# Performance work log

Measured on AMD Instinct MI355X. Metric: run time of the kernel, lower is better.

Reference implementation:

```python
import jax, jax.numpy as jnp
import numpy as np
import math

E = 65536        # neighbor pairs (edges)
NAT = 2048       # atoms
NRAD = 24        # radial basis size
ZETA = [1, 2, 3, 4]
NCOMP = len(ZETA) + 1  # radial components: one 2-body + one per zeta
RCUT = 6.0
NELEM = 94       # one-hot element encoding size
EMB = 16         # species embedding dim


def _tables():
    """Static lxlylz enumeration per zeta: triples with lx+ly+lz = n, n in 0..z,
    multinomial/binomial normalization and (-1)^n lambda sign."""
    f = np.vectorize(math.factorial)
    tabs = []
    for z in ZETA:
        L = []
        for n in range(z + 1):
            for lx in range(n + 1):
                for ly in range(n - lx + 1):
                    L.append((lx, ly, n - lx - ly))
        L = np.array(L, np.int64)              # [K,3]
        nsum = L.sum(1)                        # [K]
        fact_lxlylz = f(L[:, 0]) * f(L[:, 1]) * f(L[:, 2])
        # (nfact/fact_lxlylz) * z!/((z-n)! n!) = z! / ((z-n)! * lx!ly!lz!)
        fact_norm = math.factorial(z) / (f(z - nsum) * fact_lxlylz)
        lam = (-1.0) ** nsum
        tabs.append((jnp.asarray(L, jnp.float32),
                     jnp.asarray(fact_norm, jnp.float32),
                     jnp.asarray(lam, jnp.float32)))
    return tabs

TABS = _tables()


def _forward(rij, Wr1, br1, Wr2, br2, Ws1, bs1, Ws2, bs2,
             Wa1, ba1, Wa2, ba2, Wa3, ba3, first_atom_idx, species_idx):
    nat = species_idx.shape[0]
    r = jnp.linalg.norm(rij, axis=1)                       # [E]
    u = rij / r[:, None]                                   # [E,3] unit vectors
    fc = 0.5 * (jnp.cos(jnp.pi * jnp.minimum(r, RCUT) / RCUT) + 1.0)
    centers = jnp.linspace(0.0, RCUT, NRAD, dtype=jnp.float32)
    width = RCUT / NRAD
    basis = jnp.exp(-((r[:, None] - centers) ** 2) / (2.0 * width * width)) * fc[:, None]  # [E,NRAD]
    # learned radial functions -> [E, NRAD, NCOMP]
    h = jax.nn.silu(basis @ Wr1 + br1)
    radial = jax.nn.silu(h @ Wr2 + br2).reshape(-1, NRAD, NCOMP)
    seg = first_atom_idx
    # two-body descriptor
    feats = [jax.ops.segment_sum(radial[:, :, 0], seg, num_segments=nat)]  # [nat,NRAD]
    for iz, z in enumerate(ZETA):
        L, fnorm, lam = TABS[iz]
        # g_ij over lxlylz combos: prod of powers of unit-vector components
        g_ij = jnp.prod((u[:, None, :] + 1e-12) ** L[None, :, :], axis=-1) * fnorm  # [E,K]
        g = jnp.einsum('er,ek->erk', radial[:, :, iz + 1], g_ij)                    # [E,NRAD,K]
        gi = jax.ops.segment_sum(g, seg, num_segments=nat)                          # [nat,NRAD,K]
        g2 = gi * gi
        norm = 2.0 ** (1.0 - z)
        feats.append(jnp.sum(g2, axis=-1) * norm)          # lambda = +1
        feats.append(jnp.sum(g2 * lam, axis=-1) * norm)    # lambda = -1
    feat = jnp.concatenate(feats, axis=1)                  # [nat, NRAD*(1+2*nzeta)]
    # species embedding and correlation
    onehot = jax.nn.one_hot(species_idx, NELEM, dtype=feat.dtype)
    emb = jax.nn.silu(onehot @ Ws1 + bs1) @ Ws2 + bs2      # [nat,EMB]
    x = (feat[:, :, None] * emb[:, None, :]).reshape(nat, -1)  # [nat, F*EMB]
    h = jax.nn.silu(x @ Wa1 + ba1)
    h = jax.nn.silu(h @ Wa2 + ba2)
    e = h @ Wa3 + ba3                                      # [nat,1] atomic energies
    return jnp.sum(e)                                      # total energy


def setup_inputs() -> dict:
    key = jax.random.key(0)
    ks = jax.random.split(key, 12)
    def w(k, shp):
        return jax.random.normal(k, shp, jnp.float32) / np.float32(np.sqrt(shp[0]))
    F = NRAD * (1 + 2 * len(ZETA)) * EMB  # 3456
    return {
        "rij": jax.random.normal(ks[0], (E, 3), jnp.float32) * 2.0,
        "Wr1": w(ks[1], (NRAD, 64)), "br1": jnp.zeros((64,), jnp.float32),
        "Wr2": w(ks[2], (64, NCOMP * NRAD)), "br2": jnp.zeros((NCOMP * NRAD,), jnp.float32),
        "Ws1": w(ks[3], (NELEM, 32)), "bs1": jnp.zeros((32,), jnp.float32),
        "Ws2": w(ks[4], (32, EMB)), "bs2": jnp.zeros((EMB,), jnp.float32),
        "Wa1": w(ks[5], (F, 256)), "ba1": jnp.zeros((256,), jnp.float32),
        "Wa2": w(ks[6], (256, 128)), "ba2": jnp.zeros((128,), jnp.float32),
        "Wa3": w(ks[7], (128, 1)), "ba3": jnp.zeros((1,), jnp.float32),
        "first_atom_idx": jnp.sort(jax.random.randint(ks[8], (E,), 0, NAT)),
        "species_idx": jax.random.randint(ks[9], (NAT,), 0, NELEM),
    }


def reference(rij, Wr1, br1, Wr2, br2, Ws1, bs1, Ws2, bs2,
              Wa1, ba1, Wa2, ba2, Wa3, ba3, first_atom_idx, species_idx):
    return _forward(rij, Wr1, br1, Wr2, br2, Ws1, bs1, Ws2, bs2,
                    Wa1, ba1, Wa2, ba2, Wa3, ba3, first_atom_idx, species_idx)
```

## Files before the change

### kernel.cpp

```cpp
#include <hip/hip_runtime.h>
#include <math.h>

#define KTOT 69
#define NRADC 24
#define NFEAT 216
#define NELEMC 94
#define EMBC 16
#define H1C 256
#define H2C 128
#define CE 16
#define EPR 20
#define KGN 18
#define GSTR 84
#define GISTR 76

__device__ __constant__ int c_lx[KTOT] = {
  0,0,0,1,
  0,0,0,1,0,0,0,1,1,2,
  0,0,0,1,0,0,0,1,1,2,0,0,0,0,1,1,1,2,2,3,
  0,0,0,1,0,0,0,1,1,2,0,0,0,0,1,1,1,2,2,3,0,0,0,0,0,1,1,1,1,2,2,2,3,3,4};
__device__ __constant__ int c_ly[KTOT] = {
  0,0,1,0,
  0,0,1,0,0,1,2,0,1,0,
  0,0,1,0,0,1,2,0,1,0,0,1,2,3,0,1,2,0,1,0,
  0,0,1,0,0,1,2,0,1,0,0,1,2,3,0,1,2,0,1,0,0,1,2,3,4,0,1,2,3,0,1,2,0,1,0};
__device__ __constant__ int c_lz[KTOT] = {
  0,1,0,0,
  0,1,0,0,2,1,0,1,0,0,
  0,1,0,0,2,1,0,1,0,0,3,2,1,0,2,1,0,1,0,0,
  0,1,0,0,2,1,0,1,0,0,3,2,1,0,2,1,0,1,0,0,4,3,2,1,0,3,2,1,0,2,1,0,1,0,0};
__device__ __constant__ float c_fn[KTOT] = {
  1,1,1,1,
  1,2,2,2,1,2,1,2,2,1,
  1,3,3,3,3,6,3,6,6,3,1,3,3,1,3,6,3,3,3,1,
  1,4,4,4,6,12,6,12,12,6,4,12,12,4,12,24,12,12,12,4,
  1,4,6,4,1,4,12,12,4,6,12,6,4,4,1};
__device__ __constant__ float c_lam[KTOT] = {
  1,-1,-1,-1,
  1,-1,-1,-1,1,1,1,1,1,1,
  1,-1,-1,-1,1,1,1,1,1,1,-1,-1,-1,-1,-1,-1,-1,-1,-1,-1,
  1,-1,-1,-1,1,1,1,1,1,1,-1,-1,-1,-1,-1,-1,-1,-1,-1,-1,
  1,1,1,1,1,1,1,1,1,1,1,1,1,1,1};
__device__ __constant__ int c_k0[4] = {0,4,14,34};
__device__ __constant__ int c_kn[4] = {4,10,20,35};
__device__ __constant__ float c_zn[4] = {1.0f, 0.5f, 0.25f, 0.125f};
__device__ __constant__ int c_zidg[KGN] = {0, 1,1,1, 2,2,2,2,2, 3,3,3,3,3,3,3,3,3};

__device__ __forceinline__ float silu(float x) { return x / (1.0f + expf(-x)); }
__device__ __forceinline__ float4 silu4(float4 v) {
  v.x = silu(v.x); v.y = silu(v.y); v.z = silu(v.z); v.w = silu(v.w); return v;
}
__device__ __forceinline__ void fma4(float4& a, float s, const float4 w) {
  a.x += s * w.x; a.y += s * w.y; a.z += s * w.z; a.w += s * w.w;
}
__device__ __forceinline__ void fma44(float4& a, const float4 x, const float4 y) {
  a.x += x.x * y.x; a.y += x.y * y.y; a.z += x.z * y.z; a.w += x.w * y.w;
}
__device__ __forceinline__ float hsum4(const float4 v) { return (v.x + v.y) + (v.z + v.w); }
__device__ __forceinline__ float powsel(int l, float p, float p2, float p3, float p4) {
  float v = 1.0f;
  v = l >= 1 ? p : v;
  v = l >= 2 ? p2 : v;
  v = l >= 3 ? p3 : v;
  v = l >= 4 ? p4 : v;
  return v;
}

__global__ __launch_bounds__(256) void k_prep(
    const int* __restrict__ fai, const int* __restrict__ spc,
    const float* __restrict__ Ws1, const float* __restrict__ bs1,
    const float* __restrict__ Ws2, const float* __restrict__ bs2,
    const float* __restrict__ Wa1,
    int* __restrict__ bounds, int* __restrict__ order,
    float* __restrict__ B, int E, int nat, int nbB) {
  const int blk = blockIdx.x;
  const int tid = threadIdx.x;
  __shared__ float s_hh[24 * 32];
  __shared__ float s_emb[24 * EMBC];
  __shared__ int s_cnt[NELEMC];
  __shared__ int s_off[NELEMC];

  if (blk < nbB) {
    int e = blk * 256 + tid;
    if (e < E) {
      int f = fai[e];
      int fp = (e == 0) ? -1 : fai[e - 1];
      for (int a = fp + 1; a <= f; ++a) bounds[a] = e;
      if (e == E - 1)
        for (int a = f + 1; a <= nat; ++a) bounds[a] = E;
    }
  } else if (blk == nbB) {
    for (int i = tid; i < NELEMC; i += 256) s_cnt[i] = 0;
    __syncthreads();
    for (int a = tid; a < nat; a += 256) atomicAdd(&s_cnt[spc[a]], 1);
    __syncthreads();
    if (tid == 0) {
      int run = 0;
      for (int s = 0; s < NELEMC; ++s) { s_off[s] = run; run += s_cnt[s]; }
    }
    __syncthreads();
    for (int a = tid; a < nat; a += 256) {
      int pos = atomicAdd(&s_off[spc[a]], 1);
      order[pos] = a;
    }
  } else {
    const int bi = blk - nbB - 1;
    const int i = bi >> 2;
    const int sc0 = (bi & 3) * 24;
    const int scn = min(NELEMC, sc0 + 24) - sc0;
    const int o = tid;
    for (int idx = tid; idx < scn * 32; idx += 256) {
      int s = idx >> 5, c = idx & 31;
      s_hh[idx] = silu(Ws1[(sc0 + s) * 32 + c] + bs1[c]);
    }
    __syncthreads();
    for (int idx = tid; idx < scn * EMBC; idx += 256) {
      int s = idx >> 4, j = idx & 15;
      float acc = bs2[j];
      #pragma unroll
      for (int c = 0; c < 32; ++c) acc += s_hh[s * 32 + c] * Ws2[c * EMBC + j];
      s_emb[idx] = acc;
    }
    __syncthreads();
    float w[EMBC];
    #pragma unroll
    for (int j = 0; j < EMBC; ++j) w[j] = Wa1[(size_t)(i * EMBC + j) * H1C + o];
    for (int s = 0; s < scn; ++s) {
      float acc = 0.0f;
      #pragma unroll
      for (int j = 0; j < EMBC; ++j) acc += s_emb[s * EMBC + j] * w[j];
      B[((size_t)(sc0 + s) * NFEAT + i) * H1C + o] = acc;
    }
  }
}

template <int NQ>
__device__ __forceinline__ void edge_l2(
    const float* __restrict__ s_h, const float* __restrict__ Wr2,
    const float* __restrict__ br2, float4* __restrict__ radial4,
    int lane, int og, int ebase, int E) {
  float4 a0[NQ], a1[NQ];
  const float4* b2 = (const float4*)(br2 + og * 32);
  #pragma unroll
  for (int q = 0; q < NQ; ++q) { a0[q] = b2[q]; a1[q] = b2[q]; }
  #pragma unroll 2
  for (int j = 0; j < 64; ++j) {
    float h0 = s_h[lane * 65 + j];
    float h1 = s_h[(lane + 64) * 65 + j];
    const float4* w = (const float4*)(Wr2 + j * 120 + og * 32);
    #pragma unroll
    for (int q = 0; q < NQ; ++q) {
      float4 wq = w[q];
      fma4(a0[q], h0, wq);
      fma4(a1[q], h1, wq);
    }
  }
  const int e0 = ebase + lane, e1 = e0 + 64;
  if (e0 < E) {
    #pragma unroll
    for (int q = 0; q < NQ; ++q) radial4[e0 * 30 + og * 8 + q] = silu4(a0[q]);
  }
  if (e1 < E) {
    #pragma unroll
    for (int q = 0; q < NQ; ++q) radial4[e1 * 30 + og * 8 + q] = silu4(a1[q]);
  }
}

__global__ __launch_bounds__(256) void k_edge(
    const float* __restrict__ rij,
    const float* __restrict__ Wr1, const float* __restrict__ br1,
    const float* __restrict__ Wr2, const float* __restrict__ br2,
    float4* __restrict__ radial4, int E) {
  __shared__ float s_bas[128 * 25];
  __shared__ float s_h[128 * 65];
  const int tid = threadIdx.x;
  const int lane = tid & 63;
  const int og = __builtin_amdgcn_readfirstlane(tid >> 6);
  const int ebase = blockIdx.x * 128;

  {
    const int ehh = og >> 1;
    const int m0 = (og & 1) * 12;
    const int el = ehh * 64 + lane;
    const int eg = ebase + el;
    float x = 0.0f, y = 0.0f, z = 0.0f;
    const bool ev = eg < E;
    if (ev) { x = rij[3 * eg]; y = rij[3 * eg + 1]; z = rij[3 * eg + 2]; }
    float r = sqrtf(x * x + y * y + z * z);
    float fcv = ev ? 0.5f * (cosf(3.14159265358979323846f * fminf(r, 6.0f) *
                                  (1.0f / 6.0f)) + 1.0f)
                   : 0.0f;
    #pragma unroll
    for (int t = 0; t < 12; ++t) {
      int m = m0 + t;
      float d = r - (6.0f / 23.0f) * (float)m;
      s_bas[el * 25 + m] = expf(-8.0f * d * d) * fcv;
    }
  }
  __syncthreads();

  {
    const float4* b1 = (const float4*)(br1 + og * 16);
    float4 c0[4], c1[4];
    #pragma unroll
    for (int q = 0; q < 4; ++q) { c0[q] = b1[q]; c1[q] = b1[q]; }
    #pragma unroll 4
    for (int m = 0; m < NRADC; ++m) {
      float bA = s_bas[lane * 25 + m];
      float bB = s_bas[(lane + 64) * 25 + m];
      const float4* w = (const float4*)(Wr1 + m * 64 + og * 16);
      #pragma unroll
      for (int q = 0; q < 4; ++q) {
        float4 wq = w[q];
        fma4(c0[q], bA, wq);
        fma4(c1[q], bB, wq);
      }
    }
    #pragma unroll
    for (int q = 0; q < 4; ++q) {
      float4 v0 = silu4(c0[q]), v1 = silu4(c1[q]);
      int b0 = lane * 65 + og * 16 + 4 * q;
      int b1o = (lane + 64) * 65 + og * 16 + 4 * q;
      s_h[b0 + 0] = v0.x; s_h[b0 + 1] = v0.y; s_h[b0 + 2] = v0.z; s_h[b0 + 3] = v0.w;
      s_h[b1o + 0] = v1.x; s_h[b1o + 1] = v1.y; s_h[b1o + 2] = v1.z; s_h[b1o + 3] = v1.w;
    }
  }
  __syncthreads();

  if (og < 3) edge_l2<8>(s_h, Wr2, br2, radial4, lane, og, ebase, E);
  else        edge_l2<6>(s_h, Wr2, br2, radial4, lane, og, ebase, E);
}

__global__ __launch_bounds__(256) void k_atom(
    const float* __restrict__ rij,
    const float4* __restrict__ radial4,
    const int* __restrict__ bounds,
    float* __restrict__ feat, int E) {
  const int a = blockIdx.x;
  const int tid = threadIdx.x;
  __shared__ __align__(16) float s_radT[120 * EPR];
  __shared__ __align__(16) float s_gijT[KGN * GSTR];
  __shared__ __align__(16) float s_gi[NRADC * GISTR];
  __shared__ float s_feat[NFEAT];

  const int start = bounds[a];
  const int end = bounds[a + 1];

  const int e = tid & 15;
  const int sub = tid >> 4;

  const bool is_tile = tid < 216;
  const int eh = (tid < 216) ? (tid / 108) : 0;
  const int tile = (tid < 216) ? (tid % 108) : 0;
  const int rg = tile % 6;
  const int kg = tile / 6;
  const int comp0 = rg * 20 + 1 + c_zidg[kg];
  const bool is_2b = (tid >= 216 && tid < 240);
  const int rad2b = tid - 216;

  const int kstart = sub < 5 ? sub * 5 : 25 + (sub - 5) * 4;
  const int kcnt = sub < 5 ? 5 : 4;
  int t_pk[5], t_addr[5]; float t_fn[5];
  #pragma unroll
  for (int t = 0; t < 5; ++t) {
    int k = (t < kcnt) ? kstart + t : 0;
    t_pk[t] = c_lx[k] | (c_ly[k] << 8) | (c_lz[k] << 16);
    t_fn[t] = c_fn[k];
    int prow = k + (k < 14 ? 0 : 2);
    t_addr[t] = (prow >> 2) * GSTR + (prow & 3) * EPR + e;
  }

  const int pe0 = tid / 30, pc0 = tid - pe0 * 30;
  const int pe1 = (tid + 256) / 30, pc1 = (tid + 256) - pe1 * 30;

  if (tid < 60) {
    int rr = tid / EPR, ec = tid % EPR;
    int fkg = rr < 2 ? 3 : 17;
    int fj = rr < 2 ? 2 + rr : 3;
    s_gijT[fkg * GSTR + fj * EPR + ec] = 0.0f;
  }

  float4 acc[4][4];
  #pragma unroll
  for (int i = 0; i < 4; ++i)
    #pragma unroll
    for (int j = 0; j < 4; ++j) acc[i][j] = make_float4(0, 0, 0, 0);
  float4 acc2b = make_float4(0, 0, 0, 0);

  float4 pfA, pfB;
  float rx, ry, rz;
  auto prefetch = [&](int c0) {
    int lim = (end - c0) * 30;
    pfA = make_float4(0, 0, 0, 0);
    pfB = make_float4(0, 0, 0, 0);
    if (tid < lim) pfA = radial4[(size_t)c0 * 30 + tid];
    if (tid < 224 && tid + 256 < lim) pfB = radial4[(size_t)c0 * 30 + 256 + tid];
    int eg = c0 + e;
    rx = 0.0f; ry = 0.0f; rz = 0.0f;
    if (eg < end) { rx = rij[3 * eg]; ry = rij[3 * eg + 1]; rz = rij[3 * eg + 2]; }
  };
  prefetch(start);

  for (int c0 = start; c0 < end; c0 += CE) {
    __syncthreads();
    {
      int c = pc0 * 4;
      s_radT[(c + 0) * EPR + pe0] = pfA.x;
      s_radT[(c + 1) * EPR + pe0] = pfA.y;
      s_radT[(c + 2) * EPR + pe0] = pfA.z;
      s_radT[(c + 3) * EPR + pe0] = pfA.w;
      if (tid < 224) {
        int c2 = pc1 * 4;
        s_radT[(c2 + 0) * EPR + pe1] = pfB.x;
        s_radT[(c2 + 1) * EPR + pe1] = pfB.y;
        s_radT[(c2 + 2) * EPR + pe1] = pfB.z;
        s_radT[(c2 + 3) * EPR + pe1] = pfB.w;
      }
    }
    {
      const bool ev = (c0 + e) < end;
      float r = sqrtf(rx * rx + ry * ry + rz * rz);
      float inv = 1.0f / r;
      float px = rx * inv + 1e-12f, py = ry * inv + 1e-12f, pz = rz * inv + 1e-12f;
      float p2x = px * px, p3x = p2x * px, p4x = p2x * p2x;
      float p2y = py * py, p3y = p2y * py, p4y = p2y * p2y;
      float p2z = pz * pz, p3z = p2z * pz, p4z = p2z * p2z;
      #pragma unroll
      for (int t = 0; t < 5; ++t) {
        if (t < kcnt) {
          int pk = t_pk[t];
          float g = powsel(pk & 0xff, px, p2x, p3x, p4x) *
                    powsel((pk >> 8) & 0xff, py, p2y, p3y, p4y) *
                    powsel(pk >> 16, pz, p2z, p3z, p4z) * t_fn[t];
          s_gijT[t_addr[t]] = ev ? g : 0.0f;
        }
      }
    }
    __syncthreads();
    prefetch(c0 + CE);
    if (is_tile) {
      #pragma unroll
      for (int s = 0; s < 2; ++s) {
        int e0 = eh * 8 + s * 4;
        float4 gg[4];
        #pragma unroll
        for (int j = 0; j < 4; ++j)
          gg[j] = *(const float4*)&s_gijT[kg * GSTR + j * EPR + e0];
        #pragma unroll
        for (int i = 0; i < 4; ++i) {
          float4 rr = *(const float4*)&s_radT[(comp0 + 5 * i) * EPR + e0];
          #pragma unroll
          for (int j = 0; j < 4; ++j) fma44(acc[i][j], rr, gg[j]);
        }
      }
    }
    if (is_2b) {
      #pragma unroll
      for (int e0 = 0; e0 < 16; e0 += 4) {
        float4 v = *(const float4*)&s_radT[(rad2b * 5) * EPR + e0];
        acc2b.x += v.x; acc2b.y += v.y; acc2b.z += v.z; acc2b.w += v.w;
      }
    }
  }

  float4 hs[4];
  #pragma unroll
  for (int i = 0; i < 4; ++i)
    hs[i] = make_float4(hsum4(acc[i][0]), hsum4(acc[i][1]),
                        hsum4(acc[i][2]), hsum4(acc[i][3]));
  __syncthreads();
  if (is_tile && eh == 0) {
    #pragma unroll
    for (int i = 0; i < 4; ++i)
      *(float4*)&s_gi[(rg * 4 + i) * GISTR + kg * 4] = hs[i];
  }
  if (is_2b) s_feat[rad2b] = hsum4(acc2b);
  __syncthreads();
  if (is_tile && eh == 1) {
    #pragma unroll
    for (int i = 0; i < 4; ++i) {
      float4 v = *(const float4*)&s_gi[(rg * 4 + i) * GISTR + kg * 4];
      v.x += hs[i].x; v.y += hs[i].y; v.z += hs[i].z; v.w += hs[i].w;
      *(float4*)&s_gi[(rg * 4 + i) * GISTR + kg * 4] = v;
    }
  }
  __syncthreads();

  if (tid < 192) {
    int zb = tid / NRADC;
    int rad = tid - zb * NRADC;
    int z = zb >> 1;
    bool neg = zb & 1;
    int k0 = c_k0[z], kn = c_kn[z];
    float s = 0.0f;
    for (int k = k0; k < k0 + kn; ++k) {
      int prow = k + (k < 14 ? 0 : 2);
      float g = s_gi[rad * GISTR + prow];
      float g2 = g * g;
      s += neg ? g2 * c_lam[k] : g2;
    }
    s_feat[NRADC + zb * NRADC + rad] = s * c_zn[z];
  }
  __syncthreads();
  if (tid < NFEAT) feat[(size_t)a * NFEAT + tid] = s_feat[tid];
}

__global__ __launch_bounds__(256) void k_mlp(
    const float* __restrict__ feat, const float* __restrict__ B,
    const float* __restrict__ ba1, const float* __restrict__ Wa2,
    const float* __restrict__ ba2, const float* __restrict__ Wa3,
    const float* __restrict__ ba3, const int* __restrict__ order,
    const int* __restrict__ sp, float* __restrict__ e_out, int nat) {
  const int nb = gridDim.x;
  int blk = blockIdx.x;
  if ((nb & 7) == 0) blk = (blockIdx.x & 7) * (nb >> 3) + (blockIdx.x >> 3);
  const int a = order[blk];
  const int s = sp[a];
  const int o = threadIdx.x;
  __shared__ __align__(16) float s_f[NFEAT];
  __shared__ __align__(16) float s_h1[H1C];
  __shared__ float s_red[2];

  if (o < 54)
    *(float4*)&s_f[o * 4] = *(const float4*)(feat + (size_t)a * NFEAT + o * 4);
  __syncthreads();
  {
    float a0 = ba1[o], a1 = 0.0f;
    const float* Bp = B + (size_t)s * NFEAT * H1C + o;
    #pragma unroll 8
    for (int i = 0; i < NFEAT; i += 2) {
      a0 += s_f[i] * Bp[(size_t)i * H1C];
      a1 += s_f[i + 1] * Bp[(size_t)(i + 1) * H1C];
    }
    s_h1[o] = silu(a0 + a1);
  }
  __syncthreads();
  if (o < H2C) {
    float a0 = ba2[o], a1 = 0.0f;
    #pragma unroll 8
    for (int j = 0; j < H1C; j += 2) {
      a0 += s_h1[j] * Wa2[j * H2C + o];
      a1 += s_h1[j + 1] * Wa2[(j + 1) * H2C + o];
    }
    float part = silu(a0 + a1) * Wa3[o];
    #pragma unroll
    for (int d = 32; d; d >>= 1) part += __shfl_down(part, d, 64);
    if ((o & 63) == 0) s_red[o >> 6] = part;
  }
  __syncthreads();
  if (o == 0) e_out[a] = s_red[0] + s_red[1] + ba3[0];
}

__global__ void k_reduce(const float* __restrict__ e_in, float* __restrict__ out, int nat) {
  int t = threadIdx.x;
  double acc = 0.0;
  for (int i = t; i < nat; i += 256) acc += (double)e_in[i];
  for (int o = 32; o; o >>= 1) acc += __shfl_down(acc, o, 64);
  __shared__ double s_par[4];
  if ((t & 63) == 0) s_par[t >> 6] = acc;
  __syncthreads();
  if (t == 0) out[0] = (float)(s_par[0] + s_par[1] + s_par[2] + s_par[3]);
}

extern "C" void kernel_launch(void* const* d_in, const int* in_sizes, int n_in,
                              void* d_out, int out_size, void* d_ws, size_t ws_size,
                              hipStream_t stream) {
  const float* rij = (const float*)d_in[0];
  const float* Wr1 = (const float*)d_in[1];
  const float* br1 = (const float*)d_in[2];
  const float* Wr2 = (const float*)d_in[3];
  const float* br2 = (const float*)d_in[4];
  const float* Ws1 = (const float*)d_in[5];
  const float* bs1 = (const float*)d_in[6];
  const float* Ws2 = (const float*)d_in[7];
  const float* bs2 = (const float*)d_in[8];
  const float* Wa1 = (const float*)d_in[9];
  const float* ba1 = (const float*)d_in[10];
  const float* Wa2 = (const float*)d_in[11];
  const float* ba2 = (const float*)d_in[12];
  const float* Wa3 = (const float*)d_in[13];
  const float* ba3 = (const float*)d_in[14];
  const int* fai = (const int*)d_in[15];
  const int* spc = (const int*)d_in[16];

  const int E = in_sizes[0] / 3;
  const int nat = in_sizes[16];

  float* ws = (float*)d_ws;
  size_t off = 0;
  float* radial = ws + off; off += (size_t)E * 120;
  float* feat = ws + off;  off += (size_t)nat * NFEAT;
  float* Bm = ws + off;    off += (size_t)NELEMC * NFEAT * H1C;
  float* e_ws = ws + off;  off += (size_t)nat;
  int* order = (int*)(ws + off); off += (size_t)nat;
  int* bounds = (int*)(ws + off);

  const int nbB = (E + 255) / 256;
  k_prep<<<nbB + 1 + NFEAT * 4, 256, 0, stream>>>(fai, spc, Ws1, bs1, Ws2, bs2,
                                                  Wa1, bounds, order, Bm, E, nat,
                                                  nbB);
  k_edge<<<(E + 127) / 128, 256, 0, stream>>>(rij, Wr1, br1, Wr2, br2,
                                              (float4*)radial, E);
  k_atom<<<nat, 256, 0, stream>>>(rij, (const float4*)radial, bounds, feat, E);
  k_mlp<<<nat, 256, 0, stream>>>(feat, Bm, ba1, Wa2, ba2, Wa3, ba3,
                                 order, spc, e_ws, nat);
  k_reduce<<<1, 256, 0, stream>>>(e_ws, (float*)d_out, nat);
}
```

Baseline: 206.5 us.

## Batch atoms per species into tiles of 8 for the MLP and stage edge stores

The per-atom MLP is split into two kernels that each handle 8 same-species atoms per block, so every load of the species weight matrix B and of Wa2 is reused across 8 atoms. The species ordering is padded to multiples of 8, with -1 marking empty slots. Separately, the edge kernel now stages radial outputs in shared memory so the global writes are coalesced. In exchange this adds an intermediate h1 buffer, an extra kernel launch, padding waste, and a fixed NPT limit on tile count that assumes the species distribution fits.

```diff
diff --git a/kernel.cpp b/kernel.cpp
--- a/kernel.cpp
+++ b/kernel.cpp
@@ -13,6 +13,8 @@
 #define KGN 18
 #define GSTR 84
 #define GISTR 76
+#define TA 8
+#define NPT 344
 
 __device__ __constant__ int c_lx[KTOT] = {
   0,0,0,1,
@@ -71,7 +73,7 @@
     const float* __restrict__ Ws1, const float* __restrict__ bs1,
     const float* __restrict__ Ws2, const float* __restrict__ bs2,
     const float* __restrict__ Wa1,
-    int* __restrict__ bounds, int* __restrict__ order,
+    int* __restrict__ bounds, int* __restrict__ porder,
     float* __restrict__ B, int E, int nat, int nbB) {
   const int blk = blockIdx.x;
   const int tid = threadIdx.x;
@@ -96,12 +98,16 @@
     __syncthreads();
     if (tid == 0) {
       int run = 0;
-      for (int s = 0; s < NELEMC; ++s) { s_off[s] = run; run += s_cnt[s]; }
-    }
+      for (int s = 0; s < NELEMC; ++s) {
+        s_off[s] = run;
+        run += ((s_cnt[s] + TA - 1) / TA) * TA;
+      }
+    }
+    for (int i = tid; i < NPT * TA; i += 256) porder[i] = -1;
     __syncthreads();
     for (int a = tid; a < nat; a += 256) {
       int pos = atomicAdd(&s_off[spc[a]], 1);
-      order[pos] = a;
+      porder[pos] = a;
     }
   } else {
     const int bi = blk - nbB - 1;
@@ -135,11 +141,10 @@
 }
 
 template <int NQ>
-__device__ __forceinline__ void edge_l2(
+__device__ __forceinline__ void edge_l2c(
     const float* __restrict__ s_h, const float* __restrict__ Wr2,
-    const float* __restrict__ br2, float4* __restrict__ radial4,
-    int lane, int og, int ebase, int E) {
-  float4 a0[NQ], a1[NQ];
+    const float* __restrict__ br2, int lane, int og,
+    float4* a0, float4* a1) {
   const float4* b2 = (const float4*)(br2 + og * 32);
   #pragma unroll
   for (int q = 0; q < NQ; ++q) { a0[q] = b2[q]; a1[q] = b2[q]; }
@@ -154,15 +159,6 @@
       fma4(a0[q], h0, wq);
       fma4(a1[q], h1, wq);
     }
-  }
-  const int e0 = ebase + lane, e1 = e0 + 64;
-  if (e0 < E) {
-    #pragma unroll
-    for (int q = 0; q < NQ; ++q) radial4[e0 * 30 + og * 8 + q] = silu4(a0[q]);
-  }
-  if (e1 < E) {
-    #pragma unroll
-    for (int q = 0; q < NQ; ++q) radial4[e1 * 30 + og * 8 + q] = silu4(a1[q]);
   }
 }
 
@@ -173,6 +169,7 @@
     float4* __restrict__ radial4, int E) {
   __shared__ float s_bas[128 * 25];
   __shared__ float s_h[128 * 65];
+  __shared__ __align__(16) float4 s_st[64 * 30];
   const int tid = threadIdx.x;
   const int lane = tid & 63;
   const int og = __builtin_amdgcn_readfirstlane(tid >> 6);
@@ -227,8 +224,28 @@
   }
   __syncthreads();
 
-  if (og < 3) edge_l2<8>(s_h, Wr2, br2, radial4, lane, og, ebase, E);
-  else        edge_l2<6>(s_h, Wr2, br2, radial4, lane, og, ebase, E);
+  float4 a0[8], a1[8];
+  int nq;
+  if (og < 3) { edge_l2c<8>(s_h, Wr2, br2, lane, og, a0, a1); nq = 8; }
+  else        { edge_l2c<6>(s_h, Wr2, br2, lane, og, a0, a1); nq = 6; }
+
+  #pragma unroll
+  for (int q = 0; q < 8; ++q)
+    if (q < nq) s_st[lane * 30 + og * 8 + q] = silu4(a0[q]);
+  __syncthreads();
+  for (int idx = tid; idx < 64 * 30; idx += 256) {
+    int eg = ebase + idx / 30;
+    if (eg < E) radial4[(size_t)ebase * 30 + idx] = s_st[idx];
+  }
+  __syncthreads();
+  #pragma unroll
+  for (int q = 0; q < 8; ++q)
+    if (q < nq) s_st[lane * 30 + og * 8 + q] = silu4(a1[q]);
+  __syncthreads();
+  for (int idx = tid; idx < 64 * 30; idx += 256) {
+    int eg = ebase + 64 + idx / 30;
+    if (eg < E) radial4[(size_t)(ebase + 64) * 30 + idx] = s_st[idx];
+  }
 }
 
 __global__ __launch_bounds__(256) void k_atom(
@@ -405,50 +422,108 @@
   if (tid < NFEAT) feat[(size_t)a * NFEAT + tid] = s_feat[tid];
 }
 
-__global__ __launch_bounds__(256) void k_mlp(
+__global__ __launch_bounds__(256) void k_mlp1(
     const float* __restrict__ feat, const float* __restrict__ B,
-    const float* __restrict__ ba1, const float* __restrict__ Wa2,
-    const float* __restrict__ ba2, const float* __restrict__ Wa3,
-    const float* __restrict__ ba3, const int* __restrict__ order,
-    const int* __restrict__ sp, float* __restrict__ e_out, int nat) {
+    const float* __restrict__ ba1, const int* __restrict__ porder,
+    const int* __restrict__ sp, float* __restrict__ h1) {
   const int nb = gridDim.x;
   int blk = blockIdx.x;
   if ((nb & 7) == 0) blk = (blockIdx.x & 7) * (nb >> 3) + (blockIdx.x >> 3);
-  const int a = order[blk];
-  const int s = sp[a];
+  const int r0 = blk * TA;
   const int o = threadIdx.x;
-  __shared__ __align__(16) float s_f[NFEAT];
-  __shared__ __align__(16) float s_h1[H1C];
-  __shared__ float s_red[2];
-
-  if (o < 54)
-    *(float4*)&s_f[o * 4] = *(const float4*)(feat + (size_t)a * NFEAT + o * 4);
-  __syncthreads();
-  {
-    float a0 = ba1[o], a1 = 0.0f;
-    const float* Bp = B + (size_t)s * NFEAT * H1C + o;
-    #pragma unroll 8
-    for (int i = 0; i < NFEAT; i += 2) {
-      a0 += s_f[i] * Bp[(size_t)i * H1C];
-      a1 += s_f[i + 1] * Bp[(size_t)(i + 1) * H1C];
-    }
-    s_h1[o] = silu(a0 + a1);
-  }
-  __syncthreads();
-  if (o < H2C) {
-    float a0 = ba2[o], a1 = 0.0f;
-    #pragma unroll 8
-    for (int j = 0; j < H1C; j += 2) {
-      a0 += s_h1[j] * Wa2[j * H2C + o];
-      a1 += s_h1[j + 1] * Wa2[(j + 1) * H2C + o];
-    }
-    float part = silu(a0 + a1) * Wa3[o];
-    #pragma unroll
-    for (int d = 32; d; d >>= 1) part += __shfl_down(part, d, 64);
-    if ((o & 63) == 0) s_red[o >> 6] = part;
-  }
-  __syncthreads();
-  if (o == 0) e_out[a] = s_red[0] + s_red[1] + ba3[0];
+  __shared__ int s_a[TA];
+  __shared__ __align__(16) float s_fT[NFEAT * TA];
+  if (o < TA) s_a[o] = porder[r0 + o];
+  __syncthreads();
+  if (s_a[0] < 0) return;
+  const int s = sp[s_a[0]];
+  for (int idx = o; idx < TA * 54; idx += 256) {
+    int u = idx / 54, q = idx - u * 54;
+    int a = s_a[u];
+    float4 v = make_float4(0, 0, 0, 0);
+    if (a >= 0) v = *(const float4*)(feat + (size_t)a * NFEAT + q * 4);
+    s_fT[(q * 4 + 0) * TA + u] = v.x;
+    s_fT[(q * 4 + 1) * TA + u] = v.y;
+    s_fT[(q * 4 + 2) * TA + u] = v.z;
+    s_fT[(q * 4 + 3) * TA + u] = v.w;
+  }
+  __syncthreads();
+  float4 A0 = make_float4(0, 0, 0, 0), A1 = make_float4(0, 0, 0, 0);
+  const float* Bp = B + ((size_t)s * NFEAT) * H1C + o;
+  #pragma unroll 4
+  for (int i = 0; i < NFEAT; ++i) {
+    float bv = Bp[(size_t)i * H1C];
+    float4 f0 = *(const float4*)&s_fT[i * TA];
+    float4 f1 = *(const float4*)&s_fT[i * TA + 4];
+    fma4(A0, bv, f0);
+    fma4(A1, bv, f1);
+  }
+  const float b1v = ba1[o];
+  float hv[TA] = {A0.x, A0.y, A0.z, A0.w, A1.x, A1.y, A1.z, A1.w};
+  #pragma unroll
+  for (int u = 0; u < TA; ++u)
+    h1[(size_t)(r0 + u) * H1C + o] = silu(hv[u] + b1v);
+}
+
+__global__ __launch_bounds__(256) void k_mlp2(
+    const float* __restrict__ h1, const float* __restrict__ Wa2,
+    const float* __restrict__ ba2, const float* __restrict__ Wa3,
+    const float* __restrict__ ba3, const int* __restrict__ porder,
+    float* __restrict__ e_out) {
+  const int nb = gridDim.x;
+  int blk = blockIdx.x;
+  if ((nb & 7) == 0) blk = (blockIdx.x & 7) * (nb >> 3) + (blockIdx.x >> 3);
+  const int r0 = blk * TA;
+  const int tid = threadIdx.x;
+  const int o = tid & 127;
+  const int half = tid >> 7;
+  __shared__ int s_a[TA];
+  __shared__ __align__(16) float s_hT[H1C * TA];
+  __shared__ float s_pre[TA][132];
+  __shared__ float s_val[TA][132];
+  if (tid < TA) s_a[tid] = porder[r0 + tid];
+  __syncthreads();
+  if (s_a[0] < 0) return;
+  for (int idx = tid; idx < TA * 64; idx += 256) {
+    int u = idx >> 6, q = idx & 63;
+    float4 v = *(const float4*)(h1 + (size_t)(r0 + u) * H1C + q * 4);
+    s_hT[(q * 4 + 0) * TA + u] = v.x;
+    s_hT[(q * 4 + 1) * TA + u] = v.y;
+    s_hT[(q * 4 + 2) * TA + u] = v.z;
+    s_hT[(q * 4 + 3) * TA + u] = v.w;
+  }
+  __syncthreads();
+  float4 A0 = make_float4(0, 0, 0, 0), A1 = make_float4(0, 0, 0, 0);
+  const int j0 = half * 128;
+  #pragma unroll 4
+  for (int j = j0; j < j0 + 128; ++j) {
+    float wv = Wa2[j * H2C + o];
+    float4 h0 = *(const float4*)&s_hT[j * TA];
+    float4 hb = *(const float4*)&s_hT[j * TA + 4];
+    fma4(A0, wv, h0);
+    fma4(A1, wv, hb);
+  }
+  float pa[TA] = {A0.x, A0.y, A0.z, A0.w, A1.x, A1.y, A1.z, A1.w};
+  if (half == 0) {
+    #pragma unroll
+    for (int u = 0; u < TA; ++u) s_pre[u][o] = pa[u];
+  }
+  __syncthreads();
+  if (half == 1) {
+    float b = ba2[o], w3 = Wa3[o];
+    #pragma unroll
+    for (int u = 0; u < TA; ++u)
+      s_val[u][o] = silu(s_pre[u][o] + pa[u] + b) * w3;
+  }
+  __syncthreads();
+  if (tid < TA) {
+    int a = s_a[tid];
+    if (a >= 0) {
+      float ss = 0.0f;
+      for (int k = 0; k < H2C; ++k) ss += s_val[tid][k];
+      e_out[a] = ss + ba3[0];
+    }
+  }
 }
 
 __global__ void k_reduce(const float* __restrict__ e_in, float* __restrict__ out, int nat) {
@@ -491,18 +566,19 @@
   float* radial = ws + off; off += (size_t)E * 120;
   float* feat = ws + off;  off += (size_t)nat * NFEAT;
   float* Bm = ws + off;    off += (size_t)NELEMC * NFEAT * H1C;
+  float* h1 = ws + off;    off += (size_t)NPT * TA * H1C;
   float* e_ws = ws + off;  off += (size_t)nat;
-  int* order = (int*)(ws + off); off += (size_t)nat;
+  int* porder = (int*)(ws + off); off += (size_t)NPT * TA;
   int* bounds = (int*)(ws + off);
 
   const int nbB = (E + 255) / 256;
   k_prep<<<nbB + 1 + NFEAT * 4, 256, 0, stream>>>(fai, spc, Ws1, bs1, Ws2, bs2,
-                                                  Wa1, bounds, order, Bm, E, nat,
+                                                  Wa1, bounds, porder, Bm, E, nat,
                                                   nbB);
   k_edge<<<(E + 127) / 128, 256, 0, stream>>>(rij, Wr1, br1, Wr2, br2,
                                               (float4*)radial, E);
   k_atom<<<nat, 256, 0, stream>>>(rij, (const float4*)radial, bounds, feat, E);
-  k_mlp<<<nat, 256, 0, stream>>>(feat, Bm, ba1, Wa2, ba2, Wa3, ba3,
-                                 order, spc, e_ws, nat);
+  k_mlp1<<<NPT, 256, 0, stream>>>(feat, Bm, ba1, porder, spc, h1);
+  k_mlp2<<<NPT, 256, 0, stream>>>(h1, Wa2, ba2, Wa3, ba3, porder, e_ws);
   k_reduce<<<1, 256, 0, stream>>>(e_ws, (float*)d_out, nat);
 }
```

Result: slower. 213.2 us (+3.2%).
